# Kernel tuning notes

Hardware: AMD Instinct MI355X
Metric: run time of the kernel (lower is better)

## Reference

```python
import jax, jax.numpy as jnp
import numpy as np


def conv2d_reflect(x, w, b, stride):
    # 3x3 conv, padding=1, padding_mode='reflect'
    x = jnp.pad(x, ((0, 0), (0, 0), (1, 1), (1, 1)), mode='reflect')
    y = jax.lax.conv_general_dilated(x, w, (stride, stride), 'VALID',
                                     dimension_numbers=('NCHW', 'OIHW', 'NCHW'))
    return y + b[None, :, None, None]


def avg_pool(x, k):
    B, C, H, W = x.shape
    return x.reshape(B, C, H // k, k, W // k, k).mean(axis=(3, 5))


def _interp_axis(x, size_out, axis):
    # 1D linear interpolation with align_corners=True semantics
    size_in = x.shape[axis]
    pos = jnp.linspace(0.0, size_in - 1.0, size_out)
    i0 = jnp.clip(jnp.floor(pos).astype(jnp.int32), 0, size_in - 2)
    frac = (pos - i0.astype(x.dtype))
    shape = [1] * x.ndim
    shape[axis] = size_out
    frac = frac.reshape(shape)
    a = jnp.take(x, i0, axis=axis)
    b = jnp.take(x, i0 + 1, axis=axis)
    return a + frac * (b - a)


def resize_bilinear_ac(x, oh, ow):
    return _interp_axis(_interp_axis(x, oh, 2), ow, 3)


def _forward(img, conv1_w, conv1_b, conv2_w, conv2_b, conv3_w, conv3_b,
             conv4_w, conv4_b, lin1_w, lin1_b, lin2_w, lin2_b, luts):
    B, C, H, W = img.shape
    silu = jax.nn.silu
    # --- feature branch on fixed 256x256 resize ---
    x = resize_bilinear_ac(img, 256, 256)
    c1 = silu(conv2d_reflect(x, conv1_w, conv1_b, 2))    # [B,32,128,128]
    c2 = silu(conv2d_reflect(c1, conv2_w, conv2_b, 2))   # [B,64,64,64]
    c3 = silu(conv2d_reflect(c2, conv3_w, conv3_b, 2))   # [B,128,32,32]
    c4 = silu(conv2d_reflect(c3, conv4_w, conv4_b, 2))   # [B,256,16,16]
    feat = jnp.concatenate([avg_pool(c1, 16), avg_pool(c2, 8),
                            avg_pool(c3, 4), avg_pool(c4, 2)], axis=1)  # [B,480,8,8]
    h1 = silu(conv2d_reflect(feat, lin1_w, lin1_b, 1))   # [B,128,8,8]
    wl = jax.lax.conv_general_dilated(h1, lin2_w, (1, 1), 'VALID',
                                      dimension_numbers=('NCHW', 'OIHW', 'NCHW'))
    wl = jax.nn.sigmoid(wl + lin2_b[None, :, None, None])  # [B,27,8,8]
    weights = resize_bilinear_ac(wl, H, W)               # [B, C*K, H, W]
    # --- adaptive 1D LUT transform (per-pixel interpolated gather) ---
    Cl, K, N = luts.shape
    pos = jnp.clip(img, 0.0, 1.0) * (N - 1)
    i0 = jnp.clip(jnp.floor(pos).astype(jnp.int32), 0, N - 2)  # [B,C,H,W]
    frac = pos - i0.astype(pos.dtype)
    cidx = jnp.arange(Cl)[None, :, None, None, None]
    kidx = jnp.arange(K)[None, None, :, None, None]
    iexp = i0[:, :, None, :, :]
    v0 = luts[cidx, kidx, iexp]          # [B,C,K,H,W]
    v1 = luts[cidx, kidx, iexp + 1]
    val = v0 + frac[:, :, None, :, :] * (v1 - v0)
    wts = weights.reshape(B, Cl, K, H, W)
    return jnp.einsum('bckhw,bckhw->bchw', wts, val)


def setup_inputs() -> dict:
    key = jax.random.key(0)
    ks = jax.random.split(key, 10)
    s = 0.05
    return {
        'img': jax.random.uniform(ks[0], (2, 3, 1024, 1024), dtype=jnp.float32),
        'conv1_w': jax.random.normal(ks[1], (32, 3, 3, 3), dtype=jnp.float32) * s,
        'conv1_b': jnp.zeros((32,), jnp.float32),
        'conv2_w': jax.random.normal(ks[2], (64, 32, 3, 3), dtype=jnp.float32) * s,
        'conv2_b': jnp.zeros((64,), jnp.float32),
        'conv3_w': jax.random.normal(ks[3], (128, 64, 3, 3), dtype=jnp.float32) * s,
        'conv3_b': jnp.zeros((128,), jnp.float32),
        'conv4_w': jax.random.normal(ks[4], (256, 128, 3, 3), dtype=jnp.float32) * s,
        'conv4_b': jnp.zeros((256,), jnp.float32),
        'lin1_w': jax.random.normal(ks[5], (128, 480, 3, 3), dtype=jnp.float32) * s,
        'lin1_b': jnp.zeros((128,), jnp.float32),
        'lin2_w': jax.random.normal(ks[6], (27, 128, 1, 1), dtype=jnp.float32) * s,
        'lin2_b': jnp.zeros((27,), jnp.float32),
        'luts': jax.random.normal(ks[7], (3, 9, 256), dtype=jnp.float32),
    }


def reference(img, conv1_w, conv1_b, conv2_w, conv2_b, conv3_w, conv3_b,
              conv4_w, conv4_b, lin1_w, lin1_b, lin2_w, lin2_b, luts):
    out = _forward(img, conv1_w, conv1_b, conv2_w, conv2_b, conv3_w, conv3_b,
                   conv4_w, conv4_b, lin1_w, lin1_b, lin2_w, lin2_b, luts)
    return jnp.clip(out, 0.0, 1.0)
```

## Files before the change

kernel.cpp:

```cpp
#include <hip/hip_runtime.h>

#define DI __device__ __forceinline__

DI float silu_f(float x) { return x / (1.f + __expf(-x)); }
DI float sigmoid_f(float x) { return 1.f / (1.f + __expf(-x)); }
DI int reflect_i(int i, int n) { if (i < 0) i = -i; if (i >= n) i = 2 * n - 2 - i; return i; }

__global__ void k_resize(const float* __restrict__ img, float* __restrict__ x) {
    int idx = blockIdx.x * blockDim.x + threadIdx.x;
    if (idx >= 2 * 3 * 256 * 256) return;
    int ox = idx & 255;
    int oy = (idx >> 8) & 255;
    int bc = idx >> 16;
    float py = oy * (1023.f / 255.f);
    float px = ox * (1023.f / 255.f);
    int iy0 = (int)floorf(py); if (iy0 > 1022) iy0 = 1022; float fy = py - (float)iy0;
    int ix0 = (int)floorf(px); if (ix0 > 1022) ix0 = 1022; float fx = px - (float)ix0;
    const float* p = img + (size_t)bc * 1024 * 1024;
    float a00 = p[iy0 * 1024 + ix0],       a01 = p[iy0 * 1024 + ix0 + 1];
    float a10 = p[(iy0 + 1) * 1024 + ix0], a11 = p[(iy0 + 1) * 1024 + ix0 + 1];
    float r0 = a00 + fy * (a10 - a00);
    float r1 = a01 + fy * (a11 - a01);
    x[idx] = r0 + fx * (r1 - r0);
}

template<int CIN, int HIN, int WIN, int COUT, int PX_PER, int OC_PER>
__global__ __launch_bounds__(256) void k_conv(const float* __restrict__ in,
                                              const float* __restrict__ w,
                                              const float* __restrict__ bias,
                                              float* __restrict__ out) {
    constexpr int HOUT = HIN / 2, WOUT = WIN / 2;
    constexpr int W_U = WOUT / PX_PER;
    constexpr int NPXU = 2 * HOUT * W_U;
    constexpr int NB_PX = NPXU / 256;
    constexpr int XSPAN = 2 * PX_PER + 1;

    __shared__ float sw[OC_PER * CIN * 9];
    const int tid = threadIdx.x;
    const int ocu = blockIdx.x / NB_PX;
    const int bpx = blockIdx.x % NB_PX;
    {
        const float* src = w + (size_t)(ocu * OC_PER) * CIN * 9;
        for (int i = tid; i < OC_PER * CIN * 9; i += 256) sw[i] = src[i];
    }
    __syncthreads();

    const int pxu = bpx * 256 + tid;
    const int oxu = pxu % W_U;
    const int oy  = (pxu / W_U) % HOUT;
    const int bb  = pxu / (W_U * HOUT);
    const int ox0 = oxu * PX_PER;

    int iy[3];
#pragma unroll
    for (int k = 0; k < 3; ++k) iy[k] = reflect_i(2 * oy + k - 1, HIN);
    int xs[XSPAN];
#pragma unroll
    for (int d = 0; d < XSPAN; ++d) xs[d] = reflect_i(2 * ox0 - 1 + d, WIN);

    float acc[OC_PER][PX_PER];
#pragma unroll
    for (int o = 0; o < OC_PER; ++o)
#pragma unroll
        for (int p = 0; p < PX_PER; ++p) acc[o][p] = 0.f;

    for (int ic = 0; ic < CIN; ++ic) {
        const float* ib = in + ((size_t)bb * CIN + ic) * HIN * WIN;
        float t[3][XSPAN];
#pragma unroll
        for (int ky = 0; ky < 3; ++ky) {
            const float* rp = ib + iy[ky] * WIN;
#pragma unroll
            for (int d = 0; d < XSPAN; ++d) t[ky][d] = rp[xs[d]];
        }
#pragma unroll
        for (int o = 0; o < OC_PER; ++o) {
            const float* wp = sw + ((size_t)o * CIN + ic) * 9;
            float wv[9];
#pragma unroll
            for (int j = 0; j < 9; ++j) wv[j] = wp[j];
#pragma unroll
            for (int p = 0; p < PX_PER; ++p)
#pragma unroll
                for (int ky = 0; ky < 3; ++ky)
#pragma unroll
                    for (int kx = 0; kx < 3; ++kx)
                        acc[o][p] = fmaf(t[ky][2 * p + kx], wv[ky * 3 + kx], acc[o][p]);
        }
    }

#pragma unroll
    for (int o = 0; o < OC_PER; ++o) {
        const int oc = ocu * OC_PER + o;
        float bv = bias[oc];
        float* op = out + (((size_t)bb * COUT + oc) * HOUT + oy) * WOUT + ox0;
        if (PX_PER == 4) {
            float4 v = make_float4(silu_f(acc[o][0] + bv), silu_f(acc[o][1] + bv),
                                   silu_f(acc[o][2] + bv), silu_f(acc[o][3] + bv));
            *(float4*)op = v;
        } else if (PX_PER == 2) {
            float2 v = make_float2(silu_f(acc[o][0] + bv), silu_f(acc[o][1] + bv));
            *(float2*)op = v;
        } else {
#pragma unroll
            for (int p = 0; p < PX_PER; ++p) op[p] = silu_f(acc[o][p] + bv);
        }
    }
}

template<int CIN, int HIN, int WIN, int COUT, int OC_PER>
__global__ __launch_bounds__(256) void k_conv_w4(const float* __restrict__ in,
                                                 const float* __restrict__ w,
                                                 const float* __restrict__ bias,
                                                 float* __restrict__ out) {
    constexpr int HOUT = HIN / 2, WOUT = WIN / 2;
    constexpr int NPXU = 2 * HOUT * WOUT;
    constexpr int NB_PX = NPXU / 64;
    constexpr int ICC = CIN / 4;

    __shared__ float sw[OC_PER * CIN * 12];
    __shared__ float sred[4][OC_PER][64];
    const int tid = threadIdx.x;
    const int ocu = blockIdx.x / NB_PX;
    const int bpx = blockIdx.x % NB_PX;
    {
        const float* src = w + (size_t)(ocu * OC_PER) * CIN * 9;
        for (int i = tid; i < OC_PER * CIN * 9; i += 256)
            sw[(i / 9) * 12 + (i % 9)] = src[i];
    }
    __syncthreads();

    const int kc = tid >> 6;
    const int lane = tid & 63;
    const int pxu = bpx * 64 + lane;
    const int ox = pxu % WOUT;
    const int oy = (pxu / WOUT) % HOUT;
    const int bb = pxu / (WOUT * HOUT);

    int iy[3], xs[3];
#pragma unroll
    for (int k = 0; k < 3; ++k) {
        iy[k] = reflect_i(2 * oy + k - 1, HIN);
        xs[k] = reflect_i(2 * ox + k - 1, WIN);
    }

    float acc[OC_PER];
#pragma unroll
    for (int o = 0; o < OC_PER; ++o) acc[o] = 0.f;

    for (int icl = 0; icl < ICC; ++icl) {
        const int ic = kc * ICC + icl;
        const float* ib = in + ((size_t)bb * CIN + ic) * HIN * WIN;
        float t[3][3];
#pragma unroll
        for (int ky = 0; ky < 3; ++ky) {
            const float* rp = ib + iy[ky] * WIN;
#pragma unroll
            for (int kx = 0; kx < 3; ++kx) t[ky][kx] = rp[xs[kx]];
        }
#pragma unroll
        for (int o = 0; o < OC_PER; ++o) {
            const float* wp = sw + ((size_t)o * CIN + ic) * 12;
            float wv[9];
#pragma unroll
            for (int j = 0; j < 9; ++j) wv[j] = wp[j];
#pragma unroll
            for (int ky = 0; ky < 3; ++ky)
#pragma unroll
                for (int kx = 0; kx < 3; ++kx)
                    acc[o] = fmaf(t[ky][kx], wv[ky * 3 + kx], acc[o]);
        }
    }

#pragma unroll
    for (int o = 0; o < OC_PER; ++o) sred[kc][o][lane] = acc[o];
    __syncthreads();
    if (kc < OC_PER) {
        const int o = kc;
        const int oc = ocu * OC_PER + o;
        float s = sred[0][o][lane] + sred[1][o][lane] + sred[2][o][lane] + sred[3][o][lane];
        out[(((size_t)bb * COUT + oc) * HOUT + oy) * WOUT + ox] = silu_f(s + bias[oc]);
    }
}

__global__ void k_pool(const float* __restrict__ c1, const float* __restrict__ c2,
                       const float* __restrict__ c3, const float* __restrict__ c4,
                       float* __restrict__ feat) {
    int idx = blockIdx.x * blockDim.x + threadIdx.x;
    if (idx >= 2 * 480 * 64) return;
    int x = idx & 7;
    int y = (idx >> 3) & 7;
    int fc = (idx >> 6) % 480;
    int bb = idx / (480 * 64);
    const float* src; int C, HW, k, c;
    if (fc < 32)       { src = c1; C = 32;  HW = 128; k = 16; c = fc; }
    else if (fc < 96)  { src = c2; C = 64;  HW = 64;  k = 8;  c = fc - 32; }
    else if (fc < 224) { src = c3; C = 128; HW = 32;  k = 4;  c = fc - 96; }
    else               { src = c4; C = 256; HW = 16;  k = 2;  c = fc - 224; }
    const float* p = src + ((size_t)bb * C + c) * HW * HW + (y * k) * HW + x * k;
    float s = 0.f;
    if (k >= 4) {
        for (int i = 0; i < k; ++i) {
            const float4* r4 = (const float4*)(p + i * HW);
            for (int j = 0; j < k / 4; ++j) {
                float4 q = r4[j];
                s += q.x + q.y + q.z + q.w;
            }
        }
    } else {
        for (int i = 0; i < k; ++i)
            for (int j = 0; j < k; ++j) s += p[i * HW + j];
    }
    feat[idx] = s / (float)(k * k);
}

__global__ __launch_bounds__(512) void k_lin1(const float* __restrict__ feat,
                                              const float* __restrict__ w,
                                              const float* __restrict__ bias,
                                              float* __restrict__ h1) {
    __shared__ float sw[480 * 9];
    __shared__ float sred[8][64];
    const int tid = threadIdx.x;
    const int bb = blockIdx.x >> 7;
    const int oc = blockIdx.x & 127;
    {
        const float* src = w + (size_t)oc * 480 * 9;
        for (int i = tid; i < 480 * 9; i += 512) sw[i] = src[i];
    }
    const int wave = tid >> 6;
    const int lane = tid & 63;
    const int py = lane >> 3, px = lane & 7;
    int srcl[9];
#pragma unroll
    for (int ky = 0; ky < 3; ++ky)
#pragma unroll
        for (int kx = 0; kx < 3; ++kx)
            srcl[ky * 3 + kx] = reflect_i(py + ky - 1, 8) * 8 + reflect_i(px + kx - 1, 8);
    __syncthreads();

    const float* fp = feat + (size_t)bb * 480 * 64;
    float acc = 0.f;
    for (int ic = wave * 60; ic < wave * 60 + 60; ++ic) {
        float v = fp[ic * 64 + lane];
        const float* wp = sw + ic * 9;
#pragma unroll
        for (int j = 0; j < 9; ++j)
            acc = fmaf(__shfl(v, srcl[j], 64), wp[j], acc);
    }
    sred[wave][lane] = acc;
    __syncthreads();
    if (wave == 0) {
        float s = 0.f;
#pragma unroll
        for (int wv = 0; wv < 8; ++wv) s += sred[wv][lane];
        h1[((size_t)bb * 128 + oc) * 64 + lane] = silu_f(s + bias[oc]);
    }
}

__global__ void k_lin2(const float* __restrict__ h1, const float* __restrict__ w,
                       const float* __restrict__ bias, float* __restrict__ wl) {
    int idx = blockIdx.x * blockDim.x + threadIdx.x;
    if (idx >= 2 * 27 * 64) return;
    int pix = idx & 63;
    int oc = (idx >> 6) % 27;
    int bb = idx / (27 * 64);
    const float* hp = h1 + (size_t)bb * 128 * 64 + pix;
    const float* wp = w + oc * 128;
    float sum = bias[oc];
    for (int ic = 0; ic < 128; ++ic) sum = fmaf(hp[ic * 64], wp[ic], sum);
    wl[((size_t)bb * 27 + oc) * 64 + pix] = sigmoid_f(sum);
}

__global__ __launch_bounds__(256) void k_apply(const float* __restrict__ img,
                                               const float* __restrict__ wl,
                                               const float* __restrict__ luts,
                                               float* __restrict__ out) {
    __shared__ float slut[9 * 256];
    __shared__ float swl[9 * 64];
    __shared__ float su[9 * 8];
    int tid = threadIdx.x;
    int bc = blockIdx.y;
    int bb = bc / 3, c = bc % 3;
    for (int i = tid; i < 9 * 256; i += 256) slut[i] = luts[c * 9 * 256 + i];
    for (int i = tid; i < 9 * 64; i += 256) swl[i] = wl[((size_t)bb * 27 + c * 9) * 64 + i];

    const size_t plane = (((size_t)bb * 3 + c) * 1024);
    int x0 = tid * 4;
    float fx[4]; int ix0[4];
#pragma unroll
    for (int p = 0; p < 4; ++p) {
        float pxf = (x0 + p) * (7.f / 1023.f);
        int i = (int)pxf; if (i > 6) i = 6;
        ix0[p] = i; fx[p] = pxf - (float)i;
    }

    for (int rr = 0; rr < 8; ++rr) {
        int h = blockIdx.x * 8 + rr;
        float py = h * (7.f / 1023.f);
        int iy0 = (int)py; if (iy0 > 6) iy0 = 6;
        float fy = py - (float)iy0;
        __syncthreads();
        if (tid < 72) {
            int k = tid >> 3, ixx = tid & 7;
            float s0 = swl[k * 64 + iy0 * 8 + ixx];
            float s1 = swl[k * 64 + iy0 * 8 + 8 + ixx];
            su[tid] = fmaf(fy, s1 - s0, s0);
        }
        __syncthreads();

        size_t base = (plane + h) * 1024;
        float4 v = ((const float4*)(img + base))[tid];
        float xin[4] = {v.x, v.y, v.z, v.w};
        float o[4];
#pragma unroll
        for (int p = 0; p < 4; ++p) {
            float pv = fminf(fmaxf(xin[p], 0.f), 1.f) * 255.f;
            int i0 = (int)pv; if (i0 > 254) i0 = 254;
            float fr = pv - (float)i0;
            float acc = 0.f;
#pragma unroll
            for (int k = 0; k < 9; ++k) {
                float s0 = su[k * 8 + ix0[p]];
                float s1 = su[k * 8 + ix0[p] + 1];
                float wt = fmaf(fx[p], s1 - s0, s0);
                float l0 = slut[k * 256 + i0];
                float l1 = slut[k * 256 + i0 + 1];
                acc = fmaf(wt, fmaf(fr, l1 - l0, l0), acc);
            }
            o[p] = fminf(fmaxf(acc, 0.f), 1.f);
        }
        ((float4*)(out + base))[tid] = make_float4(o[0], o[1], o[2], o[3]);
    }
}

extern "C" void kernel_launch(void* const* d_in, const int* in_sizes, int n_in,
                              void* d_out, int out_size, void* d_ws, size_t ws_size,
                              hipStream_t stream) {
    const float* img     = (const float*)d_in[0];
    const float* conv1_w = (const float*)d_in[1];
    const float* conv1_b = (const float*)d_in[2];
    const float* conv2_w = (const float*)d_in[3];
    const float* conv2_b = (const float*)d_in[4];
    const float* conv3_w = (const float*)d_in[5];
    const float* conv3_b = (const float*)d_in[6];
    const float* conv4_w = (const float*)d_in[7];
    const float* conv4_b = (const float*)d_in[8];
    const float* lin1_w  = (const float*)d_in[9];
    const float* lin1_b  = (const float*)d_in[10];
    const float* lin2_w  = (const float*)d_in[11];
    const float* lin2_b  = (const float*)d_in[12];
    const float* luts    = (const float*)d_in[13];
    float* out = (float*)d_out;

    float* ws = (float*)d_ws;
    float* x_rs = ws;            ws += 2 * 3 * 256 * 256;
    float* c1   = ws;            ws += 2 * 32 * 128 * 128;
    float* c2   = ws;            ws += 2 * 64 * 64 * 64;
    float* c3   = ws;            ws += 2 * 128 * 32 * 32;
    float* c4   = ws;            ws += 2 * 256 * 16 * 16;
    float* feat = ws;            ws += 2 * 480 * 8 * 8;
    float* h1   = ws;            ws += 2 * 128 * 8 * 8;
    float* wl   = ws;            ws += 2 * 27 * 8 * 8;

    const int B = 256;
    k_resize<<<(2 * 3 * 256 * 256 + B - 1) / B, B, 0, stream>>>(img, x_rs);
    k_conv<3, 256, 256, 32, 4, 2><<<512, B, 0, stream>>>(x_rs, conv1_w, conv1_b, c1);
    k_conv<32, 128, 128, 64, 2, 2><<<512, B, 0, stream>>>(c1, conv2_w, conv2_b, c2);
    k_conv_w4<64, 64, 64, 128, 2><<<2048, B, 0, stream>>>(c2, conv3_w, conv3_b, c3);
    k_conv_w4<128, 32, 32, 256, 2><<<1024, B, 0, stream>>>(c3, conv4_w, conv4_b, c4);
    k_pool<<<(2 * 480 * 64 + B - 1) / B, B, 0, stream>>>(c1, c2, c3, c4, feat);
    k_lin1<<<256, 512, 0, stream>>>(feat, lin1_w, lin1_b, h1);
    k_lin2<<<(2 * 27 * 64 + B - 1) / B, B, 0, stream>>>(h1, lin2_w, lin2_b, wl);
    dim3 agrid(128, 6);
    k_apply<<<agrid, B, 0, stream>>>(img, wl, luts, out);
}
```

Baseline: 243.0 us.

## Restructure resize, early convs, and fuse lin2 into LUT apply kernel

The resize kernel now stages the two source rows in shared memory per output row. The first two convs switch to a wave-per-output-channel layout: 64 pixels per block, each wave computing two channels, with padded weight rows. The lin2 1x1 conv plus sigmoid is folded into the apply kernel, which removes one launch and the wl buffer. The apply kernel also stores LUT entries as adjacent pairs, precomputes row-interpolated weights for all eight rows at once, and shares the column weights across the four pixels each thread handles. In exchange, every apply block recomputes its share of lin2, and the early convs now process one pixel per thread, which gives up register reuse of the input.

New measurement: 249.2 us. +2.6%, slower.

```diff
diff --git a/kernel.cpp b/kernel.cpp
--- a/kernel.cpp
+++ b/kernel.cpp
@@ -6,105 +6,91 @@
 DI float sigmoid_f(float x) { return 1.f / (1.f + __expf(-x)); }
 DI int reflect_i(int i, int n) { if (i < 0) i = -i; if (i >= n) i = 2 * n - 2 - i; return i; }
 
-__global__ void k_resize(const float* __restrict__ img, float* __restrict__ x) {
-    int idx = blockIdx.x * blockDim.x + threadIdx.x;
-    if (idx >= 2 * 3 * 256 * 256) return;
-    int ox = idx & 255;
-    int oy = (idx >> 8) & 255;
-    int bc = idx >> 16;
+__global__ __launch_bounds__(256) void k_resize(const float* __restrict__ img,
+                                                float* __restrict__ x) {
+    __shared__ float r0s[1024], r1s[1024];
+    const int oy = blockIdx.x & 255;
+    const int bc = blockIdx.x >> 8;
     float py = oy * (1023.f / 255.f);
+    int iy0 = (int)py; if (iy0 > 1022) iy0 = 1022;
+    float fy = py - (float)iy0;
+    const float* p0 = img + ((size_t)bc * 1024 + iy0) * 1024;
+    ((float4*)r0s)[threadIdx.x] = ((const float4*)p0)[threadIdx.x];
+    ((float4*)r1s)[threadIdx.x] = ((const float4*)(p0 + 1024))[threadIdx.x];
+    __syncthreads();
+    const int ox = threadIdx.x;
     float px = ox * (1023.f / 255.f);
-    int iy0 = (int)floorf(py); if (iy0 > 1022) iy0 = 1022; float fy = py - (float)iy0;
-    int ix0 = (int)floorf(px); if (ix0 > 1022) ix0 = 1022; float fx = px - (float)ix0;
-    const float* p = img + (size_t)bc * 1024 * 1024;
-    float a00 = p[iy0 * 1024 + ix0],       a01 = p[iy0 * 1024 + ix0 + 1];
-    float a10 = p[(iy0 + 1) * 1024 + ix0], a11 = p[(iy0 + 1) * 1024 + ix0 + 1];
-    float r0 = a00 + fy * (a10 - a00);
-    float r1 = a01 + fy * (a11 - a01);
-    x[idx] = r0 + fx * (r1 - r0);
-}
-
-template<int CIN, int HIN, int WIN, int COUT, int PX_PER, int OC_PER>
-__global__ __launch_bounds__(256) void k_conv(const float* __restrict__ in,
-                                              const float* __restrict__ w,
-                                              const float* __restrict__ bias,
-                                              float* __restrict__ out) {
+    int ix0 = (int)px; if (ix0 > 1022) ix0 = 1022;
+    float fx = px - (float)ix0;
+    float a00 = r0s[ix0], a01 = r0s[ix0 + 1];
+    float a10 = r1s[ix0], a11 = r1s[ix0 + 1];
+    float r0v = a00 + fy * (a10 - a00);
+    float r1v = a01 + fy * (a11 - a01);
+    x[((size_t)bc * 256 + oy) * 256 + ox] = r0v + fx * (r1v - r0v);
+}
+
+template<int CIN, int HIN, int WIN, int COUT>
+__global__ __launch_bounds__(256) void k_conv_woc(const float* __restrict__ in,
+                                                  const float* __restrict__ w,
+                                                  const float* __restrict__ bias,
+                                                  float* __restrict__ out) {
     constexpr int HOUT = HIN / 2, WOUT = WIN / 2;
-    constexpr int W_U = WOUT / PX_PER;
-    constexpr int NPXU = 2 * HOUT * W_U;
-    constexpr int NB_PX = NPXU / 256;
-    constexpr int XSPAN = 2 * PX_PER + 1;
-
-    __shared__ float sw[OC_PER * CIN * 9];
+    constexpr int NPXU = 2 * HOUT * WOUT;
+    constexpr int NB_PX = NPXU / 64;
+
+    __shared__ float sw[8 * CIN * 12];
     const int tid = threadIdx.x;
     const int ocu = blockIdx.x / NB_PX;
     const int bpx = blockIdx.x % NB_PX;
     {
-        const float* src = w + (size_t)(ocu * OC_PER) * CIN * 9;
-        for (int i = tid; i < OC_PER * CIN * 9; i += 256) sw[i] = src[i];
-    }
-    __syncthreads();
-
-    const int pxu = bpx * 256 + tid;
-    const int oxu = pxu % W_U;
-    const int oy  = (pxu / W_U) % HOUT;
-    const int bb  = pxu / (W_U * HOUT);
-    const int ox0 = oxu * PX_PER;
-
-    int iy[3];
-#pragma unroll
-    for (int k = 0; k < 3; ++k) iy[k] = reflect_i(2 * oy + k - 1, HIN);
-    int xs[XSPAN];
-#pragma unroll
-    for (int d = 0; d < XSPAN; ++d) xs[d] = reflect_i(2 * ox0 - 1 + d, WIN);
-
-    float acc[OC_PER][PX_PER];
-#pragma unroll
-    for (int o = 0; o < OC_PER; ++o)
-#pragma unroll
-        for (int p = 0; p < PX_PER; ++p) acc[o][p] = 0.f;
-
+        const float* src = w + (size_t)(ocu * 8) * CIN * 9;
+        for (int i = tid; i < 8 * CIN * 9; i += 256)
+            sw[(i / 9) * 12 + (i % 9)] = src[i];
+    }
+    __syncthreads();
+
+    const int wave = tid >> 6, lane = tid & 63;
+    const int pxu = bpx * 64 + lane;
+    const int ox = pxu % WOUT;
+    const int oy = (pxu / WOUT) % HOUT;
+    const int bb = pxu / (WOUT * HOUT);
+
+    int iy[3], xs[3];
+#pragma unroll
+    for (int k = 0; k < 3; ++k) {
+        iy[k] = reflect_i(2 * oy + k - 1, HIN);
+        xs[k] = reflect_i(2 * ox + k - 1, WIN);
+    }
+
+    float acc[2] = {0.f, 0.f};
     for (int ic = 0; ic < CIN; ++ic) {
         const float* ib = in + ((size_t)bb * CIN + ic) * HIN * WIN;
-        float t[3][XSPAN];
+        float t[3][3];
 #pragma unroll
         for (int ky = 0; ky < 3; ++ky) {
             const float* rp = ib + iy[ky] * WIN;
 #pragma unroll
-            for (int d = 0; d < XSPAN; ++d) t[ky][d] = rp[xs[d]];
-        }
-#pragma unroll
-        for (int o = 0; o < OC_PER; ++o) {
-            const float* wp = sw + ((size_t)o * CIN + ic) * 9;
+            for (int kx = 0; kx < 3; ++kx) t[ky][kx] = rp[xs[kx]];
+        }
+#pragma unroll
+        for (int o = 0; o < 2; ++o) {
+            const float* wp = sw + ((size_t)(wave * 2 + o) * CIN + ic) * 12;
             float wv[9];
 #pragma unroll
             for (int j = 0; j < 9; ++j) wv[j] = wp[j];
 #pragma unroll
-            for (int p = 0; p < PX_PER; ++p)
-#pragma unroll
-                for (int ky = 0; ky < 3; ++ky)
-#pragma unroll
-                    for (int kx = 0; kx < 3; ++kx)
-                        acc[o][p] = fmaf(t[ky][2 * p + kx], wv[ky * 3 + kx], acc[o][p]);
-        }
-    }
-
-#pragma unroll
-    for (int o = 0; o < OC_PER; ++o) {
-        const int oc = ocu * OC_PER + o;
-        float bv = bias[oc];
-        float* op = out + (((size_t)bb * COUT + oc) * HOUT + oy) * WOUT + ox0;
-        if (PX_PER == 4) {
-            float4 v = make_float4(silu_f(acc[o][0] + bv), silu_f(acc[o][1] + bv),
-                                   silu_f(acc[o][2] + bv), silu_f(acc[o][3] + bv));
-            *(float4*)op = v;
-        } else if (PX_PER == 2) {
-            float2 v = make_float2(silu_f(acc[o][0] + bv), silu_f(acc[o][1] + bv));
-            *(float2*)op = v;
-        } else {
-#pragma unroll
-            for (int p = 0; p < PX_PER; ++p) op[p] = silu_f(acc[o][p] + bv);
-        }
+            for (int ky = 0; ky < 3; ++ky)
+#pragma unroll
+                for (int kx = 0; kx < 3; ++kx)
+                    acc[o] = fmaf(t[ky][kx], wv[ky * 3 + kx], acc[o]);
+        }
+    }
+
+#pragma unroll
+    for (int o = 0; o < 2; ++o) {
+        const int oc = ocu * 8 + wave * 2 + o;
+        out[(((size_t)bb * COUT + oc) * HOUT + oy) * WOUT + ox] =
+            silu_f(acc[o] + bias[oc]);
     }
 }
 
@@ -257,79 +243,99 @@
     }
 }
 
-__global__ void k_lin2(const float* __restrict__ h1, const float* __restrict__ w,
-                       const float* __restrict__ bias, float* __restrict__ wl) {
-    int idx = blockIdx.x * blockDim.x + threadIdx.x;
-    if (idx >= 2 * 27 * 64) return;
-    int pix = idx & 63;
-    int oc = (idx >> 6) % 27;
-    int bb = idx / (27 * 64);
-    const float* hp = h1 + (size_t)bb * 128 * 64 + pix;
-    const float* wp = w + oc * 128;
-    float sum = bias[oc];
-    for (int ic = 0; ic < 128; ++ic) sum = fmaf(hp[ic * 64], wp[ic], sum);
-    wl[((size_t)bb * 27 + oc) * 64 + pix] = sigmoid_f(sum);
-}
-
 __global__ __launch_bounds__(256) void k_apply(const float* __restrict__ img,
-                                               const float* __restrict__ wl,
+                                               const float* __restrict__ h1,
+                                               const float* __restrict__ l2w,
+                                               const float* __restrict__ l2b,
                                                const float* __restrict__ luts,
                                                float* __restrict__ out) {
-    __shared__ float slut[9 * 256];
+    __shared__ float2 slut2[9 * 256];
     __shared__ float swl[9 * 64];
-    __shared__ float su[9 * 8];
-    int tid = threadIdx.x;
-    int bc = blockIdx.y;
-    int bb = bc / 3, c = bc % 3;
-    for (int i = tid; i < 9 * 256; i += 256) slut[i] = luts[c * 9 * 256 + i];
-    for (int i = tid; i < 9 * 64; i += 256) swl[i] = wl[((size_t)bb * 27 + c * 9) * 64 + i];
-
-    const size_t plane = (((size_t)bb * 3 + c) * 1024);
-    int x0 = tid * 4;
-    float fx[4]; int ix0[4];
-#pragma unroll
-    for (int p = 0; p < 4; ++p) {
-        float pxf = (x0 + p) * (7.f / 1023.f);
-        int i = (int)pxf; if (i > 6) i = 6;
-        ix0[p] = i; fx[p] = pxf - (float)i;
-    }
-
-    for (int rr = 0; rr < 8; ++rr) {
+    __shared__ float su8[8 * 72];
+    const int tid = threadIdx.x;
+    const int bc = blockIdx.y;
+    const int bb = bc / 3, c = bc % 3;
+
+    for (int i = tid; i < 9 * 256; i += 256) {
+        int k = i >> 8, j = i & 255;
+        const float* lp = luts + (size_t)(c * 9 + k) * 256;
+        float v0 = lp[j];
+        float v1 = lp[j < 255 ? j + 1 : 255];
+        slut2[i] = make_float2(v0, v1);
+    }
+    {
+        const float* hp = h1 + (size_t)bb * 128 * 64;
+        const int pix = tid & 63;
+        for (int o = tid >> 6; o < 9; o += 4) {
+            const float* wp = l2w + (size_t)(c * 9 + o) * 128;
+            float s = l2b[c * 9 + o];
+            for (int ic = 0; ic < 128; ++ic) s = fmaf(hp[ic * 64 + pix], wp[ic], s);
+            swl[o * 64 + pix] = sigmoid_f(s);
+        }
+    }
+    __syncthreads();
+    for (int i = tid; i < 576; i += 256) {
+        int rr = i / 72, rem = i % 72;
+        int k = rem >> 3, xx = rem & 7;
         int h = blockIdx.x * 8 + rr;
         float py = h * (7.f / 1023.f);
         int iy0 = (int)py; if (iy0 > 6) iy0 = 6;
         float fy = py - (float)iy0;
-        __syncthreads();
-        if (tid < 72) {
-            int k = tid >> 3, ixx = tid & 7;
-            float s0 = swl[k * 64 + iy0 * 8 + ixx];
-            float s1 = swl[k * 64 + iy0 * 8 + 8 + ixx];
-            su[tid] = fmaf(fy, s1 - s0, s0);
-        }
-        __syncthreads();
-
-        size_t base = (plane + h) * 1024;
+        float a = swl[k * 64 + iy0 * 8 + xx];
+        float b = swl[k * 64 + iy0 * 8 + 8 + xx];
+        su8[i] = fmaf(fy, b - a, a);
+    }
+    __syncthreads();
+
+    const int x0 = tid * 4;
+    float fx[4]; int sel[4]; int cbase;
+    {
+        float p0 = x0 * (7.f / 1023.f);
+        int ib = (int)p0; if (ib > 6) ib = 6;
+        cbase = ib;
+#pragma unroll
+        for (int p = 0; p < 4; ++p) {
+            float pxf = (x0 + p) * (7.f / 1023.f);
+            int i = (int)pxf; if (i > 6) i = 6;
+            sel[p] = i - cbase;
+            fx[p] = pxf - (float)i;
+        }
+    }
+    const size_t plane = ((size_t)bb * 3 + c) * 1024;
+
+    for (int rr = 0; rr < 8; ++rr) {
+        const int h = blockIdx.x * 8 + rr;
+        const size_t base = (plane + h) * 1024;
         float4 v = ((const float4*)(img + base))[tid];
         float xin[4] = {v.x, v.y, v.z, v.w};
-        float o[4];
+        int i0[4]; float fr[4]; float acc[4] = {0.f, 0.f, 0.f, 0.f};
 #pragma unroll
         for (int p = 0; p < 4; ++p) {
             float pv = fminf(fmaxf(xin[p], 0.f), 1.f) * 255.f;
-            int i0 = (int)pv; if (i0 > 254) i0 = 254;
-            float fr = pv - (float)i0;
-            float acc = 0.f;
-#pragma unroll
-            for (int k = 0; k < 9; ++k) {
-                float s0 = su[k * 8 + ix0[p]];
-                float s1 = su[k * 8 + ix0[p] + 1];
-                float wt = fmaf(fx[p], s1 - s0, s0);
-                float l0 = slut[k * 256 + i0];
-                float l1 = slut[k * 256 + i0 + 1];
-                acc = fmaf(wt, fmaf(fr, l1 - l0, l0), acc);
+            int i = (int)pv; if (i > 254) i = 254;
+            i0[p] = i; fr[p] = pv - (float)i;
+        }
+        const float* srow = su8 + rr * 72;
+#pragma unroll
+        for (int k = 0; k < 9; ++k) {
+            float s0 = srow[k * 8 + cbase];
+            float s1 = srow[k * 8 + cbase + 1];
+            float s2 = (cbase < 6) ? srow[k * 8 + cbase + 2] : s1;
+            const float2* lrow = slut2 + k * 256;
+#pragma unroll
+            for (int p = 0; p < 4; ++p) {
+                float a = sel[p] ? s1 : s0;
+                float b = sel[p] ? s2 : s1;
+                float wt = fmaf(fx[p], b - a, a);
+                float2 l = lrow[i0[p]];
+                acc[p] = fmaf(wt, fmaf(fr[p], l.y - l.x, l.x), acc[p]);
             }
-            o[p] = fminf(fmaxf(acc, 0.f), 1.f);
-        }
-        ((float4*)(out + base))[tid] = make_float4(o[0], o[1], o[2], o[3]);
+        }
+        float4 o4 = make_float4(fminf(fmaxf(acc[0], 0.f), 1.f),
+                                fminf(fmaxf(acc[1], 0.f), 1.f),
+                                fminf(fmaxf(acc[2], 0.f), 1.f),
+                                fminf(fmaxf(acc[3], 0.f), 1.f));
+        ((float4*)(out + base))[tid] = o4;
     }
 }
 
@@ -360,17 +366,15 @@
     float* c4   = ws;            ws += 2 * 256 * 16 * 16;
     float* feat = ws;            ws += 2 * 480 * 8 * 8;
     float* h1   = ws;            ws += 2 * 128 * 8 * 8;
-    float* wl   = ws;            ws += 2 * 27 * 8 * 8;
 
     const int B = 256;
-    k_resize<<<(2 * 3 * 256 * 256 + B - 1) / B, B, 0, stream>>>(img, x_rs);
-    k_conv<3, 256, 256, 32, 4, 2><<<512, B, 0, stream>>>(x_rs, conv1_w, conv1_b, c1);
-    k_conv<32, 128, 128, 64, 2, 2><<<512, B, 0, stream>>>(c1, conv2_w, conv2_b, c2);
+    k_resize<<<6 * 256, B, 0, stream>>>(img, x_rs);
+    k_conv_woc<3, 256, 256, 32><<<2048, B, 0, stream>>>(x_rs, conv1_w, conv1_b, c1);
+    k_conv_woc<32, 128, 128, 64><<<1024, B, 0, stream>>>(c1, conv2_w, conv2_b, c2);
     k_conv_w4<64, 64, 64, 128, 2><<<2048, B, 0, stream>>>(c2, conv3_w, conv3_b, c3);
     k_conv_w4<128, 32, 32, 256, 2><<<1024, B, 0, stream>>>(c3, conv4_w, conv4_b, c4);
     k_pool<<<(2 * 480 * 64 + B - 1) / B, B, 0, stream>>>(c1, c2, c3, c4, feat);
     k_lin1<<<256, 512, 0, stream>>>(feat, lin1_w, lin1_b, h1);
-    k_lin2<<<(2 * 27 * 64 + B - 1) / B, B, 0, stream>>>(h1, lin2_w, lin2_b, wl);
     dim3 agrid(128, 6);
-    k_apply<<<agrid, B, 0, stream>>>(img, wl, luts, out);
-}
+    k_apply<<<agrid, B, 0, stream>>>(img, h1, lin2_w, lin2_b, luts, out);
+}
```
